# Performance work log

Hardware: AMD Instinct MI355X
Metric: run time of the kernel (lower is better)

Reference implementation:

```python
import jax, jax.numpy as jnp
import numpy as np

# TrafficXLSTM defaults + xlstm-library internal defaults
D = 128          # embedding_dim
INNER = 256      # mLSTM proj_factor=2 -> inner dim
NH = 4           # mLSTM heads
DHM = INNER // NH
NB = INNER // 4  # qkv_proj_blocksize=4 -> block-diagonal 4x4 blocks
SNH = 4          # sLSTM heads
SDH = D // SNH
FF = 192         # gated FFN up dim: 1.3*128 rounded up to multiple of 64
K = 4            # causal conv kernel size
EPS = 1e-6
BLOCK_TYPES = ['m', 's', 'm', 's', 'm', 'm']  # slstm_at=[1,3], num_blocks=6
B, S, IN_SIZE, OUT_SIZE = 64, 256, 3, 3


def _ln(x, w):  # LayerNorm, weight only (xlstm default bias=False)
    mu = x.mean(-1, keepdims=True)
    var = x.var(-1, keepdims=True)
    return (x - mu) * jax.lax.rsqrt(var + EPS) * w


def _mh_norm(x, w):  # MultiHeadLayerNorm: per-head groupnorm. x: (B,S,NH,dh), w: (NH*dh,)
    mu = x.mean(-1, keepdims=True)
    var = x.var(-1, keepdims=True)
    xn = (x - mu) * jax.lax.rsqrt(var + EPS)
    b, s = x.shape[:2]
    return xn.reshape(b, s, -1) * w


def _causal_conv(x, w, b):  # depthwise causal conv1d. x: (B,S,C), w: (C,K), b: (C,)
    s = x.shape[1]
    xp = jnp.pad(x, ((0, 0), (K - 1, 0), (0, 0)))
    out = b
    for k in range(K):  # fixed small kernel
        out = out + xp[:, k:k + s, :] * w[:, k]
    return out


def _headwise(x, w):  # block-diagonal linear (LinearHeadwiseExpand). x: (B,S,INNER), w: (NB,4,4)
    b, s, _ = x.shape
    xb = x.reshape(b, s, NB, 4)
    return jnp.einsum('bsnk,nkl->bsnl', xb, w).reshape(b, s, -1)


def _mlstm_layer(x, Wup, cw, cb, Wq, Wk, Wv, Wig, big, Wfg, bfg, gnw, skip, Wdown):
    b, s, _ = x.shape
    up = x @ Wup                          # (B,S,2*INNER)
    x_m, z = up[..., :INNER], up[..., INNER:]
    xc = jax.nn.silu(_causal_conv(x_m, cw, cb))
    q = _headwise(xc, Wq)
    k = _headwise(xc, Wk)
    v = _headwise(x_m, Wv)
    qkv = jnp.concatenate([q, k, v], -1)  # gates read concat(q,k,v)
    ig = (qkv @ Wig + big).transpose(0, 2, 1)  # (B,NH,S)
    fg = (qkv @ Wfg + bfg).transpose(0, 2, 1)
    qh = q.reshape(b, s, NH, DHM).transpose(0, 2, 1, 3)  # (B,NH,S,dh)
    kh = k.reshape(b, s, NH, DHM).transpose(0, 2, 1, 3)
    vh = v.reshape(b, s, NH, DHM).transpose(0, 2, 1, 3)
    # parallel stabilized mLSTM (matrix-memory, vanilla backend math)
    logf = jax.nn.log_sigmoid(fg)
    cs = jnp.cumsum(logf, -1)
    logfg = cs[..., :, None] - cs[..., None, :]          # sum_{t=j+1..i} log f_t
    mask = jnp.tril(jnp.ones((s, s), bool))
    logD = jnp.where(mask, logfg + ig[..., None, :], -1e30)
    maxD = logD.max(-1, keepdims=True)
    Dm = jnp.exp(logD - maxD)
    scores = jnp.einsum('bhid,bhjd->bhij', qh, kh) * (DHM ** -0.5)
    C = scores * Dm
    n = jnp.maximum(jnp.abs(C.sum(-1, keepdims=True)), jnp.exp(-maxD)) + EPS
    h = jnp.einsum('bhij,bhjd->bhid', C / n, vh)         # (B,NH,S,dh)
    h = h.transpose(0, 2, 1, 3)                          # (B,S,NH,dh)
    hn = _mh_norm(h, gnw)
    out = (hn + skip * xc) * jax.nn.silu(z)              # learnable skip + output gate
    return out @ Wdown


def _slstm_layer(x, cw, cb, Wg, bg, R, gnw):
    b, s, _ = x.shape
    xc = jax.nn.silu(_causal_conv(x, cw, cb))

    def gate_in(inp, w, bias):  # block-diagonal headwise gate projection
        xb = inp.reshape(b, s, SNH, SDH)
        return jnp.einsum('bsnk,nkl->bsnl', xb, w) + bias.reshape(SNH, SDH)

    gi = gate_in(xc, Wg[0], bg[0])  # i,f gates read conv output
    gf = gate_in(xc, Wg[1], bg[1])
    gz = gate_in(x, Wg[2], bg[2])   # z,o gates read raw input
    go = gate_in(x, Wg[3], bg[3])
    gates = jnp.stack([gi, gf, gz, go], 0)       # (4,B,S,NH,dh)
    gates = jnp.moveaxis(gates, 2, 0)            # (S,4,B,NH,dh)

    def step(carry, g):
        c, n, h, m = carry                       # each (B,NH,dh)
        rec = jnp.einsum('bnk,gnkl->gbnl', h, R)  # block-diag recurrent contribution
        ir, fr = g[0] + rec[0], g[1] + rec[1]
        zr, orr = g[2] + rec[2], g[3] + rec[3]
        mnew = jnp.maximum(fr + m, ir)           # stabilizer state
        i = jnp.exp(ir - mnew)
        f = jnp.exp(fr + m - mnew)
        zt = jnp.tanh(zr)
        o = jax.nn.sigmoid(orr)
        cn = f * c + i * zt
        nn = f * n + i
        hn = o * cn / (nn + 1e-8)
        return (cn, nn, hn, mnew), hn

    z0 = jnp.zeros((b, SNH, SDH), x.dtype)
    _, ys = jax.lax.scan(step, (z0, z0, z0, z0), gates)
    ys = jnp.moveaxis(ys, 0, 1)                  # (B,S,NH,dh)
    return _mh_norm(ys, gnw)


def _ffn(x, Wup, Wdown):  # gated FFN of the sLSTM block
    u = x @ Wup
    g, v = u[..., :FF], u[..., FF:]
    return (jax.nn.gelu(g) * v) @ Wdown


def _forward(x, W_emb, b_emb, m_ln_w, m_Wup, m_conv_w, m_conv_b, m_Wq, m_Wk, m_Wv,
             m_Wig, m_big, m_Wfg, m_bfg, m_gn_w, m_skip, m_Wdown,
             s_ln_w, s_conv_w, s_conv_b, s_Wg, s_bg, s_R, s_gn_w, s_ln2_w,
             s_Wff_up, s_Wff_down, post_ln_w, W_out, b_out):
    h = x @ W_emb + b_emb  # input embedding (dropout = identity in eval)
    mi = si = 0
    for bt in BLOCK_TYPES:
        if bt == 'm':  # mLSTM block: x + mlstm(LN(x))
            h = h + _mlstm_layer(_ln(h, m_ln_w[mi]), m_Wup[mi], m_conv_w[mi], m_conv_b[mi],
                                 m_Wq[mi], m_Wk[mi], m_Wv[mi], m_Wig[mi], m_big[mi],
                                 m_Wfg[mi], m_bfg[mi], m_gn_w[mi], m_skip[mi], m_Wdown[mi])
            mi += 1
        else:          # sLSTM block: x + slstm(LN(x)); x + ffn(LN(x))
            h = h + _slstm_layer(_ln(h, s_ln_w[si]), s_conv_w[si], s_conv_b[si],
                                 s_Wg[si], s_bg[si], s_R[si], s_gn_w[si])
            h = h + _ffn(_ln(h, s_ln2_w[si]), s_Wff_up[si], s_Wff_down[si])
            si += 1
    h = _ln(h, post_ln_w)
    out = h[:, -1, :] @ W_out + b_out
    return out[:, None, :]  # (B, prediction_length=1, output_size)


def setup_inputs() -> dict:
    key = jax.random.key(0)
    ks = iter(jax.random.split(key, 64))

    def w(shape, fan_in):
        return jax.random.normal(next(ks), shape, jnp.float32) / np.sqrt(fan_in)

    nm, ns = 4, 2  # number of mLSTM / sLSTM blocks
    s_bg = jnp.zeros((ns, 4, D)).at[:, 1, :].set(3.0)  # positive forget-gate bias init
    return {
        'x': jax.random.normal(next(ks), (B, S, IN_SIZE), jnp.float32),
        'W_emb': w((IN_SIZE, D), IN_SIZE), 'b_emb': jnp.zeros((D,)),
        'm_ln_w': jnp.ones((nm, D)),
        'm_Wup': w((nm, D, 2 * INNER), D),
        'm_conv_w': w((nm, INNER, K), K), 'm_conv_b': jnp.zeros((nm, INNER)),
        'm_Wq': w((nm, NB, 4, 4), 4), 'm_Wk': w((nm, NB, 4, 4), 4), 'm_Wv': w((nm, NB, 4, 4), 4),
        'm_Wig': w((nm, 3 * INNER, NH), 3 * INNER), 'm_big': jnp.zeros((nm, NH)),
        'm_Wfg': w((nm, 3 * INNER, NH), 3 * INNER),
        'm_bfg': jnp.tile(jnp.linspace(3.0, 6.0, NH), (nm, 1)),
        'm_gn_w': jnp.ones((nm, INNER)), 'm_skip': jnp.ones((nm, INNER)),
        'm_Wdown': w((nm, INNER, D), INNER),
        's_ln_w': jnp.ones((ns, D)),
        's_conv_w': w((ns, D, K), K), 's_conv_b': jnp.zeros((ns, D)),
        's_Wg': w((ns, 4, SNH, SDH, SDH), SDH), 's_bg': s_bg,
        's_R': w((ns, 4, SNH, SDH, SDH), SDH),
        's_gn_w': jnp.ones((ns, D)), 's_ln2_w': jnp.ones((ns, D)),
        's_Wff_up': w((ns, D, 2 * FF), D), 's_Wff_down': w((ns, FF, D), FF),
        'post_ln_w': jnp.ones((D,)),
        'W_out': w((D, OUT_SIZE), D), 'b_out': jnp.zeros((OUT_SIZE,)),
    }


def reference(x, W_emb, b_emb, m_ln_w, m_Wup, m_conv_w, m_conv_b, m_Wq, m_Wk, m_Wv,
              m_Wig, m_big, m_Wfg, m_bfg, m_gn_w, m_skip, m_Wdown,
              s_ln_w, s_conv_w, s_conv_b, s_Wg, s_bg, s_R, s_gn_w, s_ln2_w,
              s_Wff_up, s_Wff_down, post_ln_w, W_out, b_out):
    return _forward(x, W_emb, b_emb, m_ln_w, m_Wup, m_conv_w, m_conv_b, m_Wq, m_Wk, m_Wv,
                    m_Wig, m_big, m_Wfg, m_bfg, m_gn_w, m_skip, m_Wdown,
                    s_ln_w, s_conv_w, s_conv_b, s_Wg, s_bg, s_R, s_gn_w, s_ln2_w,
                    s_Wff_up, s_Wff_down, post_ln_w, W_out, b_out)
```

## Files before the change

### kernel.cpp

```cpp
#include <hip/hip_runtime.h>
#include <hip/hip_bf16.h>

#define D_MODEL 128
#define INNER 256
#define NH 4
#define DHM 64
#define SNH 4
#define SDH 32
#define FF 192
#define CK 4
#define BATCH 64
#define SEQ 256
#define T_TOK (BATCH*SEQ)

typedef __hip_bfloat16 bf16;

__device__ __forceinline__ float sigf(float x){ return 1.0f/(1.0f+__expf(-x)); }
__device__ __forceinline__ float bcast_lane(float v, int k){
    return __uint_as_float(__builtin_amdgcn_readlane(__float_as_uint(v), k));
}
__device__ __forceinline__ float frcp(float x){ return __builtin_amdgcn_rcpf(x); }

__global__ void sentinel_kernel(float* __restrict__ out, float v)
{
    int idx = threadIdx.x;
    if (idx < BATCH*3) out[idx] = v;
}

__global__ void embed_kernel(const float* __restrict__ x, const float* __restrict__ W,
                             const float* __restrict__ bias, float* __restrict__ h)
{
    int idx = blockIdx.x*blockDim.x + threadIdx.x;
    if (idx >= T_TOK*D_MODEL) return;
    int d = idx & 127; int t = idx >> 7;
    float s = bias[d];
    #pragma unroll
    for (int i = 0; i < 3; ++i) s += x[t*3+i] * W[i*D_MODEL+d];
    h[idx] = s;
}

__global__ void ln_kernel(const float* __restrict__ x, const float* __restrict__ w,
                          float* __restrict__ out)
{
    int t = blockIdx.x; int lane = threadIdx.x;
    float v0 = x[(size_t)t*128 + lane], v1 = x[(size_t)t*128 + 64 + lane];
    float s = v0 + v1, ss = v0*v0 + v1*v1;
    #pragma unroll
    for (int off = 32; off >= 1; off >>= 1){ s += __shfl_xor(s,off); ss += __shfl_xor(ss,off); }
    float mu  = s * (1.f/128.f);
    float var = fmaxf(ss * (1.f/128.f) - mu*mu, 0.f);
    float r   = rsqrtf(var + 1e-6f);
    out[(size_t)t*128 + lane]      = (v0-mu)*r*w[lane];
    out[(size_t)t*128 + 64 + lane] = (v1-mu)*r*w[64+lane];
}

#define TM 64
#define TN 64
#define TK 32
__global__ void __launch_bounds__(256)
gemm_tiled_kernel(const float* __restrict__ A, const float* __restrict__ W,
                  float* __restrict__ C, int M, int N, int Kd, int acc)
{
    int ntiles = N / TN;
    int bx = blockIdx.x % ntiles;
    int by = blockIdx.x / ntiles;
    __shared__ float As[TK][TM+1];
    __shared__ float Ws[TK][TN];
    int tid = threadIdx.x;
    int tn = (tid & 15) * 4;
    int tm = (tid >> 4) * 4;
    float accr[4][4] = {{0.f}};
    for (int k0 = 0; k0 < Kd; k0 += TK){
        #pragma unroll
        for (int i = tid; i < TM*TK; i += 256){
            int c2 = i & 31, r = i >> 5;
            As[c2][r] = A[(size_t)(by*TM + r)*Kd + k0 + c2];
        }
        #pragma unroll
        for (int i = tid; i < TK*TN; i += 256){
            int c2 = i & 63, r = i >> 6;
            Ws[r][c2] = W[(size_t)(k0 + r)*N + bx*TN + c2];
        }
        __syncthreads();
        #pragma unroll
        for (int k = 0; k < TK; ++k){
            float a0 = As[k][tm], a1 = As[k][tm+1], a2 = As[k][tm+2], a3 = As[k][tm+3];
            float4 wv = *(const float4*)&Ws[k][tn];
            accr[0][0] = fmaf(a0, wv.x, accr[0][0]); accr[0][1] = fmaf(a0, wv.y, accr[0][1]);
            accr[0][2] = fmaf(a0, wv.z, accr[0][2]); accr[0][3] = fmaf(a0, wv.w, accr[0][3]);
            accr[1][0] = fmaf(a1, wv.x, accr[1][0]); accr[1][1] = fmaf(a1, wv.y, accr[1][1]);
            accr[1][2] = fmaf(a1, wv.z, accr[1][2]); accr[1][3] = fmaf(a1, wv.w, accr[1][3]);
            accr[2][0] = fmaf(a2, wv.x, accr[2][0]); accr[2][1] = fmaf(a2, wv.y, accr[2][1]);
            accr[2][2] = fmaf(a2, wv.z, accr[2][2]); accr[2][3] = fmaf(a2, wv.w, accr[2][3]);
            accr[3][0] = fmaf(a3, wv.x, accr[3][0]); accr[3][1] = fmaf(a3, wv.y, accr[3][1]);
            accr[3][2] = fmaf(a3, wv.z, accr[3][2]); accr[3][3] = fmaf(a3, wv.w, accr[3][3]);
        }
        __syncthreads();
    }
    #pragma unroll
    for (int i = 0; i < 4; ++i){
        size_t off = (size_t)(by*TM + tm + i)*N + bx*TN + tn;
        if (acc){
            float4 old = *(float4*)&C[off];
            old.x += accr[i][0]; old.y += accr[i][1];
            old.z += accr[i][2]; old.w += accr[i][3];
            *(float4*)&C[off] = old;
        } else {
            *(float4*)&C[off] = make_float4(accr[i][0], accr[i][1], accr[i][2], accr[i][3]);
        }
    }
}

#define HM 128
#define HN 64
#define HK 32
__global__ void __launch_bounds__(256)
gemm_tiled_m128_kernel(const float* __restrict__ A, const float* __restrict__ W,
                       float* __restrict__ C, int M, int N, int Kd, int acc)
{
    int ntiles = N / HN;
    int bx = blockIdx.x % ntiles;
    int by = blockIdx.x / ntiles;
    __shared__ float As[HK][HM+4];
    __shared__ float Ws[HK][HN];
    int tid = threadIdx.x;
    int tn = (tid & 15) * 4;
    int tm = (tid >> 4) * 8;
    float accr[8][4] = {{0.f}};
    for (int k0 = 0; k0 < Kd; k0 += HK){
        #pragma unroll
        for (int i = tid; i < HM*HK; i += 256){
            int c2 = i & 31, r = i >> 5;
            As[c2][r] = A[(size_t)(by*HM + r)*Kd + k0 + c2];
        }
        #pragma unroll
        for (int i = tid; i < HK*HN; i += 256){
            int c2 = i & 63, r = i >> 6;
            Ws[r][c2] = W[(size_t)(k0 + r)*N + bx*HN + c2];
        }
        __syncthreads();
        #pragma unroll
        for (int k = 0; k < HK; ++k){
            float4 a0 = *(const float4*)&As[k][tm];
            float4 a1 = *(const float4*)&As[k][tm+4];
            float4 wv = *(const float4*)&Ws[k][tn];
            float av[8] = {a0.x,a0.y,a0.z,a0.w,a1.x,a1.y,a1.z,a1.w};
            #pragma unroll
            for (int ii = 0; ii < 8; ++ii){
                accr[ii][0] = fmaf(av[ii], wv.x, accr[ii][0]);
                accr[ii][1] = fmaf(av[ii], wv.y, accr[ii][1]);
                accr[ii][2] = fmaf(av[ii], wv.z, accr[ii][2]);
                accr[ii][3] = fmaf(av[ii], wv.w, accr[ii][3]);
            }
        }
        __syncthreads();
    }
    #pragma unroll
    for (int i = 0; i < 8; ++i){
        size_t off = (size_t)(by*HM + tm + i)*N + bx*HN + tn;
        if (acc){
            float4 old = *(float4*)&C[off];
            old.x += accr[i][0]; old.y += accr[i][1];
            old.z += accr[i][2]; old.w += accr[i][3];
            *(float4*)&C[off] = old;
        } else {
            *(float4*)&C[off] = make_float4(accr[i][0], accr[i][1], accr[i][2], accr[i][3]);
        }
    }
}

__global__ void conv_silu_kernel(const float* __restrict__ in, int istride,
                                 const float* __restrict__ w, const float* __restrict__ bias,
                                 float* __restrict__ out, int C)
{
    int idx = blockIdx.x*blockDim.x + threadIdx.x;
    if (idx >= T_TOK*C) return;
    int c = idx % C; int t = idx / C;
    int s = t & (SEQ-1); int b = t >> 8;
    float a = bias[c];
    int j0 = (s >= CK-1) ? s-(CK-1) : 0;
    for (int j = j0; j <= s; ++j){
        int k = j - s + (CK-1);
        a += in[(size_t)(b*SEQ+j)*istride + c] * w[c*CK + k];
    }
    out[idx] = a * sigf(a);
}

__global__ void headwise_qk_kernel(const float* __restrict__ xc,
                                   const float* __restrict__ Wq, const float* __restrict__ Wk,
                                   float* __restrict__ qout, float* __restrict__ kout)
{
    int idx = blockIdx.x*blockDim.x + threadIdx.x;
    if (idx >= T_TOK*INNER) return;
    int c = idx & 255; int t = idx >> 8;
    int n = c >> 2, l = c & 3;
    const float* xr = xc + (size_t)t*256 + n*4;
    float x0 = xr[0], x1 = xr[1], x2 = xr[2], x3 = xr[3];
    const float* wq = Wq + n*16 + l;
    const float* wk = Wk + n*16 + l;
    qout[idx] = x0*wq[0] + x1*wq[4] + x2*wq[8] + x3*wq[12];
    kout[idx] = x0*wk[0] + x1*wk[4] + x2*wk[8] + x3*wk[12];
}

__global__ void headwise_inplace_kernel(float* __restrict__ up, const float* __restrict__ W)
{
    int idx = blockIdx.x*blockDim.x + threadIdx.x;
    if (idx >= T_TOK*64) return;
    int n = idx & 63; int t = idx >> 6;
    float* xr = up + (size_t)t*512 + n*4;
    float x0 = xr[0], x1 = xr[1], x2 = xr[2], x3 = xr[3];
    const float* w = W + n*16;
    for (int l = 0; l < 4; ++l)
        xr[l] = x0*w[l] + x1*w[4+l] + x2*w[8+l] + x3*w[12+l];
}

__global__ void __launch_bounds__(256)
gateproj_kernel(const float* __restrict__ q, const float* __restrict__ k,
                const float* __restrict__ up,
                const float* __restrict__ Wig, const float* __restrict__ big,
                const float* __restrict__ Wfg, const float* __restrict__ bfg,
                float* __restrict__ igt, float* __restrict__ fgt)
{
    int t = blockIdx.x*4 + (threadIdx.x >> 6);
    int lane = threadIdx.x & 63;
    float4 si = make_float4(0.f,0.f,0.f,0.f);
    float4 sf = make_float4(0.f,0.f,0.f,0.f);
    #pragma unroll
    for (int c = 0; c < 12; ++c){
        int j = c*64 + lane;
        float xv;
        if (c < 4)      xv = q[(size_t)t*256 + j];
        else if (c < 8) xv = k[(size_t)t*256 + j - 256];
        else            xv = up[(size_t)t*512 + j - 512];
        float4 wi = *(const float4*)(Wig + (size_t)j*4);
        float4 wf = *(const float4*)(Wfg + (size_t)j*4);
        si.x = fmaf(xv, wi.x, si.x); si.y = fmaf(xv, wi.y, si.y);
        si.z = fmaf(xv, wi.z, si.z); si.w = fmaf(xv, wi.w, si.w);
        sf.x = fmaf(xv, wf.x, sf.x); sf.y = fmaf(xv, wf.y, sf.y);
        sf.z = fmaf(xv, wf.z, sf.z); sf.w = fmaf(xv, wf.w, sf.w);
    }
    #pragma unroll
    for (int off = 32; off >= 1; off >>= 1){
        si.x += __shfl_xor(si.x, off); si.y += __shfl_xor(si.y, off);
        si.z += __shfl_xor(si.z, off); si.w += __shfl_xor(si.w, off);
        sf.x += __shfl_xor(sf.x, off); sf.y += __shfl_xor(sf.y, off);
        sf.z += __shfl_xor(sf.z, off); sf.w += __shfl_xor(sf.w, off);
    }
    int b = t >> 8, s = t & 255;
    int hh = lane & 3;
    float vi = (hh==0) ? si.x : (hh==1) ? si.y : (hh==2) ? si.z : si.w;
    float vf = (hh==0) ? sf.x : (hh==1) ? sf.y : (hh==2) ? sf.z : sf.w;
    if (lane < 4)       igt[(b*4+hh)*SEQ + s] = vi + big[hh];
    else if (lane < 8)  fgt[(b*4+hh)*SEQ + s] = vf + bfg[hh];
}

__global__ void __launch_bounds__(64)
cs_kernel(const float* __restrict__ fgt, const float* __restrict__ igt,
          float* __restrict__ cs, float* __restrict__ pm)
{
    int bh = blockIdx.x;
    int lane = threadIdx.x;
    float4 f4 = *(const float4*)(fgt + (size_t)bh*SEQ + lane*4);
    float4 i4 = *(const float4*)(igt + (size_t)bh*SEQ + lane*4);
    float lf0, lf1, lf2, lf3;
    { float f = f4.x; lf0 = (f > 0.f) ? -log1pf(__expf(-f)) : f - log1pf(__expf(f)); }
    { float f = f4.y; lf1 = (f > 0.f) ? -log1pf(__expf(-f)) : f - log1pf(__expf(f)); }
    { float f = f4.z; lf2 = (f > 0.f) ? -log1pf(__expf(-f)) : f - log1pf(__expf(f)); }
    { float f = f4.w; lf3 = (f > 0.f) ? -log1pf(__expf(-f)) : f - log1pf(__expf(f)); }
    float p0 = lf0, p1 = p0 + lf1, p2 = p1 + lf2, p3 = p2 + lf3;
    float incl = p3;
    #pragma unroll
    for (int off = 1; off < 64; off <<= 1){
        float v = __shfl_up(incl, off);
        if (lane >= off) incl += v;
    }
    float excl = __shfl_up(incl, 1);
    if (lane == 0) excl = 0.f;
    float c0 = excl + p0, c1 = excl + p1, c2 = excl + p2, c3 = excl + p3;
    *(float4*)(cs + (size_t)bh*SEQ + lane*4) = make_float4(c0, c1, c2, c3);
    float u0 = i4.x - c0, u1 = i4.y - c1, u2 = i4.z - c2, u3 = i4.w - c3;
    float m0 = u0, m1 = fmaxf(m0, u1), m2 = fmaxf(m1, u2), m3 = fmaxf(m2, u3);
    float inm = m3;
    #pragma unroll
    for (int off = 1; off < 64; off <<= 1){
        float v = __shfl_up(inm, off);
        if (lane >= off) inm = fmaxf(inm, v);
    }
    float exm = __shfl_up(inm, 1);
    if (lane == 0) exm = -1e30f;
    *(float4*)(pm + (size_t)bh*SEQ + lane*4) =
        make_float4(fmaxf(exm, m0), fmaxf(exm, m1), fmaxf(exm, m2), fmaxf(exm, m3));
}

#define AC 32
#define QB 64
__global__ void __launch_bounds__(256)
attn_kernel(float* __restrict__ q, const float* __restrict__ kk,
            const float* __restrict__ up,
            const float* __restrict__ igt, const float* __restrict__ cs,
            const float* __restrict__ pm)
{
    __shared__ float k_sh[AC][DHM];
    __shared__ float v_sh[AC][DHM];
    __shared__ float S_sh[QB][33];
    __shared__ float u_sh[SEQ];
    int blk = blockIdx.x;
    int bh = blk >> 1, pair = blk & 1;
    int b = bh >> 2, hh = bh & 3;
    int tid = threadIdx.x;
    int il = tid & 63;
    int g = tid >> 6;
    u_sh[tid] = igt[bh*SEQ + tid] - cs[bh*SEQ + tid];

    for (int pass = 0; pass < 2; ++pass){
        int qt = pass ? pair : (3 - pair);
        int i = qt*QB + il;
        float csi = cs[bh*SEQ + i];
        float m   = csi + pm[bh*SEQ + i];
        const float4* qp4 = (const float4*)(q + ((size_t)(b*SEQ + i)*INNER + hh*DHM));
        float4 qr4[16];
        #pragma unroll
        for (int r = 0; r < 16; ++r) qr4[r] = qp4[r];
        float4 acc4[4];
        #pragma unroll
        for (int r = 0; r < 4; ++r) acc4[r] = make_float4(0.f,0.f,0.f,0.f);
        float ssum = 0.f;
        int cend = (qt+1)*QB;

        for (int c0 = 0; c0 < cend; c0 += AC){
            {
                int half = tid >> 7;
                int idx2 = tid & 127;
                int r0 = idx2 >> 4;
                int d4 = idx2 & 15;
                #pragma unroll
                for (int rr = 0; rr < 4; ++rr){
                    int r = r0 + rr*8;
                    size_t tj = (size_t)(b*SEQ + c0 + r);
                    if (half == 0)
                        ((float4*)&k_sh[r][0])[d4] = *(const float4*)(kk + tj*INNER + hh*DHM + d4*4);
                    else
                        ((float4*)&v_sh[r][0])[d4] = *(const float4*)(up + tj*512 + hh*DHM + d4*4);
                }
            }
            __syncthreads();
            if (i >= c0){
                #pragma unroll
                for (int jj = 0; jj < 8; ++jj){
                    int jl = g*8 + jj;
                    const float4* kr = (const float4*)&k_sh[jl][0];
                    float d0=0.f, d1=0.f, d2=0.f, d3=0.f;
                    #pragma unroll
                    for (int r4 = 0; r4 < 4; ++r4){
                        float4 ka = kr[r4*4+0], kb2 = kr[r4*4+1];
                        float4 kc = kr[r4*4+2], kd  = kr[r4*4+3];
                        float4 qa = qr4[r4*4+0], qb2 = qr4[r4*4+1];
                        float4 qc = qr4[r4*4+2], qd  = qr4[r4*4+3];
                        d0 += qa.x*ka.x + qa.y*ka.y + qa.z*ka.z + qa.w*ka.w;
                        d1 += qb2.x*kb2.x + qb2.y*kb2.y + qb2.z*kb2.z + qb2.w*kb2.w;
                        d2 += qc.x*kc.x + qc.y*kc.y + qc.z*kc.z + qc.w*kc.w;
                        d3 += qd.x*kd.x + qd.y*kd.y + qd.z*kd.z + qd.w*kd.w;
                    }
                    float dot = (d0+d1) + (d2+d3);
                    int jg = c0 + jl;
                    float arg = fminf(csi + u_sh[jg] - m, 0.f);
                    S_sh[il][jl] = (jg <= i) ? dot * 0.125f * __expf(arg) : 0.f;
                }
            }
            __syncthreads();
            if (i >= c0){
                #pragma unroll
                for (int jj = 0; jj < AC; ++jj){
                    float sv = S_sh[il][jj];
                    ssum += sv;
                    const float4* vr = (const float4*)&v_sh[jj][g*16];
                    #pragma unroll
                    for (int r = 0; r < 4; ++r){
                        float4 vv = vr[r];
                        acc4[r].x += sv*vv.x; acc4[r].y += sv*vv.y;
                        acc4[r].z += sv*vv.z; acc4[r].w += sv*vv.w;
                    }
                }
            }
            __syncthreads();
        }
        float nrm = fmaxf(fabsf(ssum), __expf(-m)) + 1e-6f;
        float rn = 1.f/nrm;
        float4* op = (float4*)(q + ((size_t)(b*SEQ + i)*INNER + hh*DHM + g*16));
        #pragma unroll
        for (int r = 0; r < 4; ++r){
            float4 o = acc4[r];
            o.x *= rn; o.y *= rn; o.z *= rn; o.w *= rn;
            op[r] = o;
        }
    }
}

__global__ void __launch_bounds__(256)
mh_gate_kernel(float* __restrict__ q, const float* __restrict__ up,
               const float* __restrict__ xc,
               const float* __restrict__ gnw, const float* __restrict__ skip)
{
    int unit = blockIdx.x*4 + (threadIdx.x >> 6);
    int lane = threadIdx.x & 63;
    int t = unit >> 2, hh = unit & 3;
    int c = hh*DHM + lane;
    float v = q[(size_t)t*256 + c];
    float s = v, ss = v*v;
    #pragma unroll
    for (int off = 32; off >= 1; off >>= 1){ s += __shfl_xor(s,off); ss += __shfl_xor(ss,off); }
    float mu  = s * (1.f/64.f);
    float var = fmaxf(ss * (1.f/64.f) - mu*mu, 0.f);
    float r   = rsqrtf(var + 1e-6f);
    float hn  = (v-mu)*r*gnw[c];
    float z   = up[(size_t)t*512 + 256 + c];
    q[(size_t)t*256 + c] = (hn + skip[c]*xc[(size_t)t*256 + c]) * (z*sigf(z));
}

#define SG_TOK 16
__global__ void __launch_bounds__(512)
slstm_gates_kernel(const float* __restrict__ xc, const float* __restrict__ xl,
                   const float* __restrict__ Wg, const float* __restrict__ bg,
                   float* __restrict__ gates)
{
    int tid = threadIdx.x;
    int l  = tid & 31;
    int gn = tid >> 5;
    int g  = gn >> 2, n = gn & 3;
    int t0 = blockIdx.x * SG_TOK;
    float wr[32];
    #pragma unroll
    for (int k = 0; k < 32; ++k) wr[k] = Wg[(size_t)gn*1024 + k*32 + l];
    float bias = bg[g*128 + n*32 + l];
    const float* xin = (g < 2) ? xc : xl;
    #pragma unroll 4
    for (int t = 0; t < SG_TOK; ++t){
        int tok = t0 + t;
        const float4* xr = (const float4*)(xin + (size_t)tok*128 + n*32);
        float a = bias;
        #pragma unroll
        for (int k4 = 0; k4 < 8; ++k4){
            float4 xv = xr[k4];
            a = fmaf(xv.x, wr[k4*4+0], a);
            a = fmaf(xv.y, wr[k4*4+1], a);
            a = fmaf(xv.z, wr[k4*4+2], a);
            a = fmaf(xv.w, wr[k4*4+3], a);
        }
        int b = tok >> 8, s = tok & 255;
        gates[(size_t)((b*4+n)*SEQ + s)*128 + l*4 + g] = a;
    }
}

__global__ void __launch_bounds__(64)
slstm_scan_kernel(const float* __restrict__ gates, const float* __restrict__ Rw,
                  float* __restrict__ ys)
{
    int bn = blockIdx.x;
    int b = bn >> 2, n = bn & 3;
    int lane = threadIdx.x;
    int l = lane & 31;
    int hi = lane >> 5;
    int gA = hi ? 2 : 0, gB = hi ? 3 : 1;
    const float* Rbase = Rw + (size_t)n*1024 + l;
    float Ra[32], Rb[32];
    #pragma unroll
    for (int k = 0; k < 32; ++k){
        Ra[k] = Rbase[(size_t)gA*4096 + k*32];
        Rb[k] = Rbase[(size_t)gB*4096 + k*32];
    }
    const float* gbase = gates + (size_t)bn*SEQ*128 + l*4 + (hi ? 2 : 0);
    float* yrow = ys + (size_t)b*SEQ*128 + n*32 + l;
    float2 cur[8], nxt[8];
    #pragma unroll
    for (int j = 0; j < 8; ++j) cur[j] = *(const float2*)(gbase + (size_t)j*128);
    float c = 0.f, nst = 0.f, m = 0.f, hst = 0.f;
    for (int ch = 0; ch < 32; ++ch){
        int nb = (ch < 31) ? (ch+1)*8 : 0;
        #pragma unroll
        for (int j = 0; j < 8; ++j)
            nxt[j] = *(const float2*)(gbase + (size_t)(nb + j)*128);
        #pragma unroll
        for (int j = 0; j < 8; ++j){
            float2 g0 = cur[j];
            float ra0=0.f, ra1=0.f, ra2=0.f, ra3=0.f;
            float rb0=0.f, rb1=0.f, rb2=0.f, rb3=0.f;
            #pragma unroll
            for (int k = 0; k < 8; ++k){
                float h0 = bcast_lane(hst, k);
                float h1 = bcast_lane(hst, k+8);
                float h2 = bcast_lane(hst, k+16);
                float h3 = bcast_lane(hst, k+24);
                ra0 = fmaf(h0, Ra[k],    ra0); rb0 = fmaf(h0, Rb[k],    rb0);
                ra1 = fmaf(h1, Ra[k+8],  ra1); rb1 = fmaf(h1, Rb[k+8],  rb1);
                ra2 = fmaf(h2, Ra[k+16], ra2); rb2 = fmaf(h2, Rb[k+16], rb2);
                ra3 = fmaf(h3, Ra[k+24], ra3); rb3 = fmaf(h3, Rb[k+24], rb3);
            }
            float ra = (ra0+ra1) + (ra2+ra3);
            float rb = (rb0+rb1) + (rb2+rb3);
            float pa = g0.x + ra;
            float pb = g0.y + rb;
            float zr  = __shfl_xor(pa, 32);
            float orr = __shfl_xor(pb, 32);
            float mnew = fmaxf(pb + m, pa);
            float iv = __expf(pa - mnew);
            float fv = __expf(pb + m - mnew);
            float zt = 1.f - 2.f*frcp(1.f + __expf(2.f*zr));
            float ov = frcp(1.f + __expf(-orr));
            c   = fv*c + iv*zt;
            nst = fv*nst + iv;
            hst = ov * c * frcp(nst + 1e-8f);
            m = mnew;
            if (!hi) yrow[(size_t)(ch*8 + j)*128] = hst;
        }
        #pragma unroll
        for (int j = 0; j < 8; ++j) cur[j] = nxt[j];
    }
}

__global__ void __launch_bounds__(256)
mh_add_kernel(const float* __restrict__ ys, const float* __restrict__ gnw,
              float* __restrict__ h)
{
    int unit = blockIdx.x*8 + (threadIdx.x >> 5);
    int l = threadIdx.x & 31;
    int t = unit >> 2, n = unit & 3;
    float v = ys[(size_t)t*128 + n*32 + l];
    float s = v, ss = v*v;
    #pragma unroll
    for (int off = 16; off >= 1; off >>= 1){ s += __shfl_xor(s,off); ss += __shfl_xor(ss,off); }
    float mu  = s * (1.f/32.f);
    float var = fmaxf(ss * (1.f/32.f) - mu*mu, 0.f);
    float r   = rsqrtf(var + 1e-6f);
    h[(size_t)t*128 + n*32 + l] += (v-mu)*r*gnw[n*32+l];
}

__global__ void geluv_kernel(const float* __restrict__ up, float* __restrict__ out)
{
    int idx = blockIdx.x*blockDim.x + threadIdx.x;
    if (idx >= T_TOK*FF) return;
    int j = idx % FF; int t = idx / FF;
    float g  = up[(size_t)t*384 + j];
    float vv = up[(size_t)t*384 + FF + j];
    float gel = 0.5f*g*(1.f + tanhf(0.7978845608028654f*(g + 0.044715f*g*g*g)));
    out[idx] = gel*vv;
}

__global__ void out_kernel(const float* __restrict__ ln, const float* __restrict__ W,
                           const float* __restrict__ bias, float* __restrict__ out)
{
    int idx = threadIdx.x;
    if (idx >= BATCH*3) return;
    int b = idx / 3, e = idx % 3;
    float s = bias[e];
    const float* xr = ln + ((size_t)(b*SEQ + SEQ-1))*128;
    for (int d = 0; d < 128; ++d) s += xr[d]*W[d*3+e];
    out[idx] = s;
}

#define LCHK do { \
    if (hipGetLastError() != hipSuccess){ \
        sentinel_kernel<<<1, 192, 0, stream>>>((float*)d_out, 3000.0f + 32.0f*(float)launch_idx); \
        return; } \
    ++launch_idx; } while(0)

extern "C" void kernel_launch(void* const* d_in, const int* in_sizes, int n_in,
                              void* d_out, int out_size, void* d_ws, size_t ws_size,
                              hipStream_t stream)
{
    (void)out_size;
    static const int expected_sizes[30] = {
        49152, 384, 128, 512, 262144, 4096, 1024, 4096, 4096, 4096,
        12288, 16, 12288, 16, 1024, 1024, 131072, 256, 1024, 256,
        32768, 1024, 32768, 256, 256, 98304, 49152, 128, 384, 3
    };
    if (n_in != 30){ sentinel_kernel<<<1,192,0,stream>>>((float*)d_out, 5000.0f); return; }
    for (int i = 0; i < 30; ++i)
        if (in_sizes[i] != expected_sizes[i]){
            sentinel_kernel<<<1,192,0,stream>>>((float*)d_out, 2000.0f + 32.0f*i); return; }
    if (ws_size < (size_t)96*1024*1024){
        sentinel_kernel<<<1,192,0,stream>>>((float*)d_out, 1000.0f + (float)(ws_size >> 20)); return; }

    const float* x        = (const float*)d_in[0];
    const float* W_emb    = (const float*)d_in[1];
    const float* b_emb    = (const float*)d_in[2];
    const float* m_ln_w   = (const float*)d_in[3];
    const float* m_Wup    = (const float*)d_in[4];
    const float* m_conv_w = (const float*)d_in[5];
    const float* m_conv_b = (const float*)d_in[6];
    const float* m_Wq     = (const float*)d_in[7];
    const float* m_Wk     = (const float*)d_in[8];
    const float* m_Wv     = (const float*)d_in[9];
    const float* m_Wig    = (const float*)d_in[10];
    const float* m_big    = (const float*)d_in[11];
    const float* m_Wfg    = (const float*)d_in[12];
    const float* m_bfg    = (const float*)d_in[13];
    const float* m_gn_w   = (const float*)d_in[14];
    const float* m_skip   = (const float*)d_in[15];
    const float* m_Wdown  = (const float*)d_in[16];
    const float* s_ln_w   = (const float*)d_in[17];
    const float* s_conv_w = (const float*)d_in[18];
    const float* s_conv_b = (const float*)d_in[19];
    const float* s_Wg     = (const float*)d_in[20];
    const float* s_bg     = (const float*)d_in[21];
    const float* s_R      = (const float*)d_in[22];
    const float* s_gn_w   = (const float*)d_in[23];
    const float* s_ln2_w  = (const float*)d_in[24];
    const float* s_Wff_up = (const float*)d_in[25];
    const float* s_Wff_dn = (const float*)d_in[26];
    const float* post_ln  = (const float*)d_in[27];
    const float* W_out    = (const float*)d_in[28];
    const float* b_out    = (const float*)d_in[29];

    float* ws  = (float*)d_ws;
    float* h   = ws;
    float* ln  = h   + (size_t)T_TOK*128;
    float* up  = ln  + (size_t)T_TOK*128;
    float* xc  = up  + (size_t)T_TOK*512;
    float* qb  = xc  + (size_t)T_TOK*256;
    float* kb  = qb  + (size_t)T_TOK*256;
    float* igt  = ln;
    float* fgt  = ln + 65536;
    float* csb  = ln + 2*65536;
    float* pmb  = ln + 3*65536;

    int launch_idx = 0;
    (void)hipGetLastError();

    embed_kernel<<<(T_TOK*128)/256, 256, 0, stream>>>(x, W_emb, b_emb, h); LCHK;

    const char* bt = "msmsmm";
    int mi = 0, si = 0;
    for (int blk = 0; blk < 6; ++blk){
        if (bt[blk] == 'm'){
            ln_kernel<<<T_TOK, 64, 0, stream>>>(h, m_ln_w + mi*128, ln); LCHK;
            gemm_tiled_m128_kernel<<<(T_TOK/HM)*(512/HN), 256, 0, stream>>>(ln, m_Wup + (size_t)mi*65536, up, T_TOK, 512, 128, 0); LCHK;
            conv_silu_kernel<<<(T_TOK*256)/256, 256, 0, stream>>>(up, 512, m_conv_w + mi*1024, m_conv_b + mi*256, xc, 256); LCHK;
            headwise_qk_kernel<<<(T_TOK*256)/256, 256, 0, stream>>>(xc, m_Wq + mi*1024, m_Wk + mi*1024, qb, kb); LCHK;
            headwise_inplace_kernel<<<(T_TOK*64)/256, 256, 0, stream>>>(up, m_Wv + mi*1024); LCHK;
            gateproj_kernel<<<T_TOK/4, 256, 0, stream>>>(qb, kb, up, m_Wig + mi*3072, m_big + mi*4,
                                                         m_Wfg + mi*3072, m_bfg + mi*4, igt, fgt); LCHK;
            cs_kernel<<<BATCH*NH, 64, 0, stream>>>(fgt, igt, csb, pmb); LCHK;
            attn_kernel<<<BATCH*NH*2, 256, 0, stream>>>(qb, kb, up, igt, csb, pmb); LCHK;
            mh_gate_kernel<<<T_TOK, 256, 0, stream>>>(qb, up, xc, m_gn_w + mi*256, m_skip + mi*256); LCHK;
            gemm_tiled_kernel<<<(T_TOK/TM)*(128/TN), 256, 0, stream>>>(qb, m_Wdown + (size_t)mi*32768, h, T_TOK, 128, 256, 1); LCHK;
            ++mi;
        } else {
            ln_kernel<<<T_TOK, 64, 0, stream>>>(h, s_ln_w + si*128, ln); LCHK;
            conv_silu_kernel<<<(T_TOK*128)/256, 256, 0, stream>>>(ln, 128, s_conv_w + si*512, s_conv_b + si*128, xc, 128); LCHK;
            slstm_gates_kernel<<<T_TOK/SG_TOK, 512, 0, stream>>>(xc, ln, s_Wg + si*16384, s_bg + si*512, up); LCHK;
            slstm_scan_kernel<<<BATCH*4, 64, 0, stream>>>(up, s_R + si*16384, kb); LCHK;
            mh_add_kernel<<<T_TOK/2, 256, 0, stream>>>(kb, s_gn_w + si*128, h); LCHK;
            ln_kernel<<<T_TOK, 64, 0, stream>>>(h, s_ln2_w + si*128, ln); LCHK;
            gemm_tiled_m128_kernel<<<(T_TOK/HM)*(384/HN), 256, 0, stream>>>(ln, s_Wff_up + (size_t)si*49152, up, T_TOK, 384, 128, 0); LCHK;
            geluv_kernel<<<(T_TOK*192)/256, 256, 0, stream>>>(up, qb); LCHK;
            gemm_tiled_kernel<<<(T_TOK/TM)*(128/TN), 256, 0, stream>>>(qb, s_Wff_dn + (size_t)si*24576, h, T_TOK, 128, 192, 1); LCHK;
            ++si;
        }
    }

    ln_kernel<<<T_TOK, 64, 0, stream>>>(h, post_ln, ln); LCHK;
    out_kernel<<<1, 192, 0, stream>>>(ln, W_out, b_out, (float*)d_out); LCHK;
}
```

Measured before the change: 1.536 ms.

## Fuse causal conv+SiLU with headwise q/k projection; widen attention key chunk

Merges the mLSTM depthwise causal conv+SiLU and the block-diagonal q/k projection into one kernel. Each thread handles one 4-channel block with float4 loads and stores, which avoids a separate launch and a re-read of xc. The attention kernel's key/value chunk grows from 32 to 64 rows, halving the chunk-loop iterations and barriers. The cost is more shared memory per block (about 49KB) and more work per thread.

```diff
diff --git a/kernel.cpp b/kernel.cpp
--- a/kernel.cpp
+++ b/kernel.cpp
@@ -186,20 +186,40 @@
     out[idx] = a * sigf(a);
 }
 
-__global__ void headwise_qk_kernel(const float* __restrict__ xc,
-                                   const float* __restrict__ Wq, const float* __restrict__ Wk,
-                                   float* __restrict__ qout, float* __restrict__ kout)
+__global__ void conv_qk_kernel(const float* __restrict__ up,
+                               const float* __restrict__ cw, const float* __restrict__ cb,
+                               const float* __restrict__ Wq, const float* __restrict__ Wk,
+                               float* __restrict__ xc, float* __restrict__ qb,
+                               float* __restrict__ kb)
 {
     int idx = blockIdx.x*blockDim.x + threadIdx.x;
-    if (idx >= T_TOK*INNER) return;
-    int c = idx & 255; int t = idx >> 8;
-    int n = c >> 2, l = c & 3;
-    const float* xr = xc + (size_t)t*256 + n*4;
-    float x0 = xr[0], x1 = xr[1], x2 = xr[2], x3 = xr[3];
-    const float* wq = Wq + n*16 + l;
-    const float* wk = Wk + n*16 + l;
-    qout[idx] = x0*wq[0] + x1*wq[4] + x2*wq[8] + x3*wq[12];
-    kout[idx] = x0*wk[0] + x1*wk[4] + x2*wk[8] + x3*wk[12];
+    if (idx >= T_TOK*64) return;
+    int n = idx & 63; int t = idx >> 6;
+    int s = t & 255, b = t >> 8;
+    float a0 = cb[n*4+0], a1 = cb[n*4+1], a2 = cb[n*4+2], a3 = cb[n*4+3];
+    int j0 = (s >= CK-1) ? s-(CK-1) : 0;
+    for (int j = j0; j <= s; ++j){
+        int k = j - s + (CK-1);
+        float4 xv = *(const float4*)(up + (size_t)(b*SEQ+j)*512 + n*4);
+        a0 = fmaf(xv.x, cw[(n*4+0)*4+k], a0);
+        a1 = fmaf(xv.y, cw[(n*4+1)*4+k], a1);
+        a2 = fmaf(xv.z, cw[(n*4+2)*4+k], a2);
+        a3 = fmaf(xv.w, cw[(n*4+3)*4+k], a3);
+    }
+    float x0 = a0*sigf(a0), x1 = a1*sigf(a1), x2 = a2*sigf(a2), x3 = a3*sigf(a3);
+    *(float4*)(xc + (size_t)t*256 + n*4) = make_float4(x0, x1, x2, x3);
+    const float* wq = Wq + n*16;
+    const float* wk = Wk + n*16;
+    float q0 = x0*wq[0] + x1*wq[4] + x2*wq[8]  + x3*wq[12];
+    float q1 = x0*wq[1] + x1*wq[5] + x2*wq[9]  + x3*wq[13];
+    float q2 = x0*wq[2] + x1*wq[6] + x2*wq[10] + x3*wq[14];
+    float q3 = x0*wq[3] + x1*wq[7] + x2*wq[11] + x3*wq[15];
+    *(float4*)(qb + (size_t)t*256 + n*4) = make_float4(q0, q1, q2, q3);
+    float k0 = x0*wk[0] + x1*wk[4] + x2*wk[8]  + x3*wk[12];
+    float k1 = x0*wk[1] + x1*wk[5] + x2*wk[9]  + x3*wk[13];
+    float k2 = x0*wk[2] + x1*wk[6] + x2*wk[10] + x3*wk[14];
+    float k3 = x0*wk[3] + x1*wk[7] + x2*wk[11] + x3*wk[15];
+    *(float4*)(kb + (size_t)t*256 + n*4) = make_float4(k0, k1, k2, k3);
 }
 
 __global__ void headwise_inplace_kernel(float* __restrict__ up, const float* __restrict__ W)
@@ -292,7 +312,7 @@
         make_float4(fmaxf(exm, m0), fmaxf(exm, m1), fmaxf(exm, m2), fmaxf(exm, m3));
 }
 
-#define AC 32
+#define AC 64
 #define QB 64
 __global__ void __launch_bounds__(256)
 attn_kernel(float* __restrict__ q, const float* __restrict__ kk,
@@ -302,7 +322,7 @@
 {
     __shared__ float k_sh[AC][DHM];
     __shared__ float v_sh[AC][DHM];
-    __shared__ float S_sh[QB][33];
+    __shared__ float S_sh[QB][AC+1];
     __shared__ float u_sh[SEQ];
     int blk = blockIdx.x;
     int bh = blk >> 1, pair = blk & 1;
@@ -334,7 +354,7 @@
                 int r0 = idx2 >> 4;
                 int d4 = idx2 & 15;
                 #pragma unroll
-                for (int rr = 0; rr < 4; ++rr){
+                for (int rr = 0; rr < 8; ++rr){
                     int r = r0 + rr*8;
                     size_t tj = (size_t)(b*SEQ + c0 + r);
                     if (half == 0)
@@ -346,8 +366,8 @@
             __syncthreads();
             if (i >= c0){
                 #pragma unroll
-                for (int jj = 0; jj < 8; ++jj){
-                    int jl = g*8 + jj;
+                for (int jj = 0; jj < 16; ++jj){
+                    int jl = g*16 + jj;
                     const float4* kr = (const float4*)&k_sh[jl][0];
                     float d0=0.f, d1=0.f, d2=0.f, d3=0.f;
                     #pragma unroll
@@ -634,8 +654,8 @@
         if (bt[blk] == 'm'){
             ln_kernel<<<T_TOK, 64, 0, stream>>>(h, m_ln_w + mi*128, ln); LCHK;
             gemm_tiled_m128_kernel<<<(T_TOK/HM)*(512/HN), 256, 0, stream>>>(ln, m_Wup + (size_t)mi*65536, up, T_TOK, 512, 128, 0); LCHK;
-            conv_silu_kernel<<<(T_TOK*256)/256, 256, 0, stream>>>(up, 512, m_conv_w + mi*1024, m_conv_b + mi*256, xc, 256); LCHK;
-            headwise_qk_kernel<<<(T_TOK*256)/256, 256, 0, stream>>>(xc, m_Wq + mi*1024, m_Wk + mi*1024, qb, kb); LCHK;
+            conv_qk_kernel<<<(T_TOK*64)/256, 256, 0, stream>>>(up, m_conv_w + mi*1024, m_conv_b + mi*256,
+                                                               m_Wq + mi*1024, m_Wk + mi*1024, xc, qb, kb); LCHK;
             headwise_inplace_kernel<<<(T_TOK*64)/256, 256, 0, stream>>>(up, m_Wv + mi*1024); LCHK;
             gateproj_kernel<<<T_TOK/4, 256, 0, stream>>>(qb, kb, up, m_Wig + mi*3072, m_big + mi*4,
                                                          m_Wfg + mi*3072, m_bfg + mi*4, igt, fgt); LCHK;
```

Result: slower. 1.767 ms (+15.0%).
